# Kernel optimization log

Hardware: AMD Instinct MI355X
Metric: run time of the kernel (lower is better)

## Reference

```python
import jax, jax.numpy as jnp
import numpy as np

# Static config (matches init_kwargs)
H, G, D = 16, 4, 128          # n_head, n_query_groups, head_size
QPK = H // G                  # queries per kv group = 4
LEFT = 1024 - 1               # sliding-window left width (local_window-1)
SCALE = 1.0 / float(np.sqrt(D))
NEG = jnp.finfo(jnp.float32).min


def _rope(x, cos, sin):
    # x: [B,T,h,D]; cos/sin: [T, D/2]; non-interleaved (flash-attn) convention
    d2 = cos.shape[-1]
    x1, x2 = x[..., :d2], x[..., d2:]
    c = cos[None, :, None, :]
    s = sin[None, :, None, :]
    return jnp.concatenate([x1 * c - x2 * s, x1 * s + x2 * c], axis=-1)


def setup_inputs() -> dict:
    key = jax.random.key(0)
    ks = jax.random.split(key, 4)
    B, T, C = 1, 2048, 2048
    x = jax.random.normal(ks[0], (B, T, C), jnp.float32)
    # real RoPE tables, base 10000
    pos = jnp.arange(T, dtype=jnp.float32)
    inv_freq = 1.0 / (10000.0 ** (jnp.arange(0, D, 2, dtype=jnp.float32) / D))
    ang = pos[:, None] * inv_freq[None, :]        # [T, D/2]
    cos, sin = jnp.cos(ang), jnp.sin(ang)
    W_attn = jax.random.normal(ks[1], ((H + 2 * G) * D, C), jnp.float32) * 0.02
    W_proj = jax.random.normal(ks[2], (C, H * D), jnp.float32) * 0.02
    k_sink = jax.random.normal(ks[3], (G * D,), jnp.float32) * 0.02
    v_sink = jnp.zeros((G * D,), jnp.float32)     # buffer, zeros in original
    return {"x": x, "cos": cos, "sin": sin, "W_attn": W_attn,
            "W_proj": W_proj, "k_sink": k_sink, "v_sink": v_sink}


def reference(x, cos, sin, W_attn, W_proj, k_sink, v_sink):
    B, T, C = x.shape
    # fused QKV projection (no bias)
    qkv = jnp.einsum('btc,oc->bto', x, W_attn)                 # [B,T,(H+2G)*D]
    qkv = qkv.reshape(B, T, G, QPK + 2, D)
    q = qkv[:, :, :, :QPK, :].reshape(B, T, H, D)              # [B,T,H,D]
    k = qkv[:, :, :, QPK, :]                                   # [B,T,G,D]
    v = qkv[:, :, :, QPK + 1, :]                               # [B,T,G,D]
    # RoPE on q and k
    q = _rope(q, cos, sin)
    k = _rope(k, cos, sin)
    # prepend sink token to k/v -> seqlen_k = T+1
    k = jnp.concatenate([jnp.broadcast_to(k_sink.reshape(1, 1, G, D), (B, 1, G, D)), k], axis=1)
    v = jnp.concatenate([jnp.broadcast_to(v_sink.reshape(1, 1, G, D), (B, 1, G, D)), v], axis=1)
    Tk = T + 1
    # GQA: group-major query head layout -> head h uses kv group h // QPK
    kh = jnp.repeat(k, QPK, axis=2)                            # [B,Tk,H,D]
    vh = jnp.repeat(v, QPK, axis=2)
    scores = jnp.einsum('bqhd,bkhd->bhqk', q, kh) * SCALE      # [B,H,T,Tk]
    # flash-attn causal + sliding window, bottom-right aligned: offset = Tk - T
    off = Tk - T
    i = jnp.arange(T)[:, None]
    j = jnp.arange(Tk)[None, :]
    allowed = (j <= i + off) & (j >= i + off - LEFT)
    scores = jnp.where(allowed[None, None], scores, NEG)
    p = jax.nn.softmax(scores, axis=-1)
    o = jnp.einsum('bhqk,bkhd->bqhd', p, vh).reshape(B, T, H * D)
    y = jnp.einsum('btd,cd->btc', o, W_proj)                   # output proj, no bias
    return y
```

## Files before the change

### kernel.cpp

```cpp
#include <hip/hip_runtime.h>

#define T_SEQ  2048
#define JP     2080
#define SL_F    0.12751744f
#define THR_L2  11.0f

typedef __attribute__((ext_vector_type(8))) short short8;
typedef __attribute__((ext_vector_type(4))) float f32x4;
typedef __attribute__((ext_vector_type(4))) int   i32x4;

__device__ __forceinline__ unsigned short f2bf(float f) {
  unsigned int u = __float_as_uint(f);
  u += 0x7fff + ((u >> 16) & 1);
  return (unsigned short)(u >> 16);
}

__device__ __forceinline__ void gload16(const void* g, void* l) {
  __builtin_amdgcn_global_load_lds(
      (const __attribute__((address_space(1))) void*)g,
      (__attribute__((address_space(3))) void*)l, 16, 0, 0);
}

__global__ __launch_bounds__(256) void quant3(
    const float* __restrict__ sx, signed char* __restrict__ dx, float* __restrict__ scx,
    const float* __restrict__ sa, signed char* __restrict__ da, float* __restrict__ sca,
    const float* __restrict__ sp, signed char* __restrict__ dp, float* __restrict__ scp) {
  __shared__ float red[4];
  int r = blockIdx.x;
  const float* s; signed char* d; float* sc; int p;
  if (r < 2048)      { s = sx; d = dx; sc = scx; p = 4194304; }
  else if (r < 5120) { r -= 2048; s = sa; d = da; sc = sca; p = 6291456; }
  else               { r -= 5120; s = sp; d = dp; sc = scp; p = 4194304; }
  const int tid = threadIdx.x;
  const float4* spv = (const float4*)(s + (size_t)r * 2048) + tid * 2;
  float4 v0 = spv[0], v1 = spv[1];
  float vv[8] = {v0.x, v0.y, v0.z, v0.w, v1.x, v1.y, v1.z, v1.w};
  float am = 0.f;
#pragma unroll
  for (int e = 0; e < 8; ++e) am = fmaxf(am, fabsf(vv[e]));
#pragma unroll
  for (int o = 1; o <= 32; o <<= 1) am = fmaxf(am, __shfl_xor(am, o, 64));
  if ((tid & 63) == 0) red[tid >> 6] = am;
  __syncthreads();
  am = fmaxf(fmaxf(red[0], red[1]), fmaxf(red[2], red[3]));
  const float inv = (am > 1e-30f) ? 32512.f / am : 0.f;
  if (tid == 0) sc[r] = am * (1.f / 32512.f);
  int hb[8], lb[8];
#pragma unroll
  for (int e = 0; e < 8; ++e) {
    int n  = __float2int_rn(vv[e] * inv);
    int nh = (n + 128) >> 8;
    hb[e] = nh & 0xff;
    lb[e] = (n - (nh << 8)) & 0xff;
  }
  int2 hw, lw;
  hw.x = hb[0] | (hb[1] << 8) | (hb[2] << 16) | (hb[3] << 24);
  hw.y = hb[4] | (hb[5] << 8) | (hb[6] << 16) | (hb[7] << 24);
  lw.x = lb[0] | (lb[1] << 8) | (lb[2] << 16) | (lb[3] << 24);
  lw.y = lb[4] | (lb[5] << 8) | (lb[6] << 16) | (lb[7] << 24);
  *(int2*)(d + (size_t)r * 2048 + tid * 8)     = hw;
  *(int2*)(d + p + (size_t)r * 2048 + tid * 8) = lw;
}

__global__ __launch_bounds__(256, 2) void gemm_i8(const signed char* __restrict__ Ag,
                                                  const signed char* __restrict__ Bg,
                                                  const float* __restrict__ sav,
                                                  const float* __restrict__ sbv,
                                                  float* __restrict__ C,
                                                  int M, int N, int K,
                                                  int kLen, int saUniform, int useAtomic) {
  __shared__ signed char Anh[2][128 * 64], Anl[2][128 * 64];
  __shared__ signed char Bnh[2][128 * 64], Bnl[2][128 * 64];

  const int tid  = threadIdx.x;
  const int lane = tid & 63;
  const int wid  = tid >> 6;
  const int wm   = (wid >> 1) << 6;
  const int wn   = (wid & 1) << 6;
  const int lo16 = lane & 15;
  const int hi4  = lane >> 4;
  const int m0   = blockIdx.y << 7;
  const int n0   = blockIdx.x << 7;
  const int kOff = blockIdx.z * kLen;
  const size_t MK = (size_t)M * K;
  const size_t NK = (size_t)N * K;

  const int r0 = (wid << 4) + (lane >> 2);
  const int r1 = r0 + 64;
  const int cB = (lane & 3) << 4;
  const signed char* a0g = Ag + (size_t)(m0 + r0) * K + cB + kOff;
  const signed char* a1g = Ag + (size_t)(m0 + r1) * K + cB + kOff;
  const signed char* b0g = Bg + (size_t)(n0 + r0) * K + cB + kOff;
  const signed char* b1g = Bg + (size_t)(n0 + r1) * K + cB + kOff;
  const int o0 = wid << 10;
  const int o1 = (4 + wid) << 10;

  int ra[4], rb[4];
#pragma unroll
  for (int i = 0; i < 4; ++i) {
    ra[i] = ((wm + i * 16 + lo16) << 6) + (hi4 << 4);
    rb[i] = ((wn + i * 16 + lo16) << 6) + (hi4 << 4);
  }

  i32x4 acc1[4][4], acc2[4][4];
  const i32x4 zi = {0, 0, 0, 0};
#pragma unroll
  for (int i = 0; i < 4; ++i)
#pragma unroll
    for (int j = 0; j < 4; ++j) { acc1[i][j] = zi; acc2[i][j] = zi; }

  gload16(a0g,      &Anh[0][o0]);
  gload16(a1g,      &Anh[0][o1]);
  gload16(a0g + MK, &Anl[0][o0]);
  gload16(a1g + MK, &Anl[0][o1]);
  gload16(b0g,      &Bnh[0][o0]);
  gload16(b1g,      &Bnh[0][o1]);
  gload16(b0g + NK, &Bnl[0][o0]);
  gload16(b1g + NK, &Bnl[0][o1]);

  int cur = 0;
  for (int k0 = 0; k0 < kLen; k0 += 64) {
    const bool more = (k0 + 64) < kLen;
    if (more) {
      const int nxt = cur ^ 1;
      const int kn  = k0 + 64;
      gload16(a0g + kn,      &Anh[nxt][o0]);
      gload16(a1g + kn,      &Anh[nxt][o1]);
      gload16(a0g + MK + kn, &Anl[nxt][o0]);
      gload16(a1g + MK + kn, &Anl[nxt][o1]);
      gload16(b0g + kn,      &Bnh[nxt][o0]);
      gload16(b1g + kn,      &Bnh[nxt][o1]);
      gload16(b0g + NK + kn, &Bnl[nxt][o0]);
      gload16(b1g + NK + kn, &Bnl[nxt][o1]);
      asm volatile("s_waitcnt vmcnt(8)" ::: "memory");
    } else {
      asm volatile("s_waitcnt vmcnt(0)" ::: "memory");
    }
    __builtin_amdgcn_s_barrier();
    __builtin_amdgcn_sched_barrier(0);

    i32x4 fah[4], fal[4], fbh[4], fbl[4];
#pragma unroll
    for (int i = 0; i < 4; ++i) {
      fah[i] = *(const i32x4*)&Anh[cur][ra[i]];
      fal[i] = *(const i32x4*)&Anl[cur][ra[i]];
      fbh[i] = *(const i32x4*)&Bnh[cur][rb[i]];
      fbl[i] = *(const i32x4*)&Bnl[cur][rb[i]];
    }
#pragma unroll
    for (int i = 0; i < 4; ++i)
#pragma unroll
      for (int j = 0; j < 4; ++j) {
        acc1[i][j] = __builtin_amdgcn_mfma_i32_16x16x64_i8(fah[i], fbh[j], acc1[i][j], 0, 0, 0);
        acc2[i][j] = __builtin_amdgcn_mfma_i32_16x16x64_i8(fah[i], fbl[j], acc2[i][j], 0, 0, 0);
        acc2[i][j] = __builtin_amdgcn_mfma_i32_16x16x64_i8(fal[i], fbh[j], acc2[i][j], 0, 0, 0);
      }

    __builtin_amdgcn_sched_barrier(0);
    __builtin_amdgcn_s_barrier();
    asm volatile("" ::: "memory");
    cur ^= 1;
  }

  const float saU = saUniform ? sav[0] : 0.f;
#pragma unroll
  for (int i = 0; i < 4; ++i) {
    const int rowb = m0 + wm + i * 16 + (hi4 << 2);
    float sa0, sa1, sa2, sa3;
    if (saUniform) { sa0 = sa1 = sa2 = sa3 = saU; }
    else { sa0 = sav[rowb]; sa1 = sav[rowb + 1]; sa2 = sav[rowb + 2]; sa3 = sav[rowb + 3]; }
#pragma unroll
    for (int j = 0; j < 4; ++j) {
      const int col = n0 + wn + j * 16 + lo16;
      const float sb = sbv[col];
      float* cp = C + (size_t)rowb * N + col;
      float v0 = fmaf(65536.f, (float)acc1[i][j][0], 256.f * (float)acc2[i][j][0]) * sa0 * sb;
      float v1 = fmaf(65536.f, (float)acc1[i][j][1], 256.f * (float)acc2[i][j][1]) * sa1 * sb;
      float v2 = fmaf(65536.f, (float)acc1[i][j][2], 256.f * (float)acc2[i][j][2]) * sa2 * sb;
      float v3 = fmaf(65536.f, (float)acc1[i][j][3], 256.f * (float)acc2[i][j][3]) * sa3 * sb;
      if (useAtomic) {
        atomicAdd(cp, v0);
        atomicAdd(cp + (size_t)N, v1);
        atomicAdd(cp + (size_t)2 * N, v2);
        atomicAdd(cp + (size_t)3 * N, v3);
      } else {
        cp[0]           = v0;
        cp[(size_t)N]   = v1;
        cp[(size_t)2*N] = v2;
        cp[(size_t)3*N] = v3;
      }
    }
  }
}

#define RB_Q  4096
#define RB_K  1024
#define RB_KE 64
#define RB_V  65

__global__ __launch_bounds__(256) void rope2(const float* __restrict__ qkv,
                                             const float* __restrict__ cosb,
                                             const float* __restrict__ sinb,
                                             const float* __restrict__ ksink,
                                             const float* __restrict__ vsink,
                                             unsigned short* __restrict__ qb,
                                             unsigned short* __restrict__ kb,
                                             unsigned short* __restrict__ vtb,
                                             float* __restrict__ vamax) {
  __shared__ unsigned short tl[512 * 33];
  __shared__ float vred[4];
  const int bid = blockIdx.x, tid = threadIdx.x;
  if (bid < RB_Q) {
    int idx = bid * 256 + tid;
    int t = idx >> 9, rem = idx & 511;
    int h = rem >> 5, dp = (rem & 31) << 1;
    int g = h >> 2, qi = h & 3;
    const float* src = qkv + (size_t)t * 3072 + g * 768 + qi * 128;
    float2 x1 = *(const float2*)(src + dp);
    float2 x2 = *(const float2*)(src + 64 + dp);
    float2 c  = *(const float2*)(cosb + t * 64 + dp);
    float2 s  = *(const float2*)(sinb + t * 64 + dp);
    ushort2 o1 = { f2bf(x1.x * c.x - x2.x * s.x), f2bf(x1.y * c.y - x2.y * s.y) };
    ushort2 o2 = { f2bf(x1.x * s.x + x2.x * c.x), f2bf(x1.y * s.y + x2.y * c.y) };
    *(ushort2*)(qb + (size_t)t * 2048 + h * 128 + dp)      = o1;
    *(ushort2*)(qb + (size_t)t * 2048 + h * 128 + 64 + dp) = o2;
  } else if (bid < RB_Q + RB_K) {
    int idx = (bid - RB_Q) * 256 + tid;
    int t = idx >> 7, rem = idx & 127;
    int g = rem >> 5, dp = (rem & 31) << 1;
    const float* src = qkv + (size_t)t * 3072 + g * 768 + 512;
    float2 x1 = *(const float2*)(src + dp);
    float2 x2 = *(const float2*)(src + 64 + dp);
    float2 c  = *(const float2*)(cosb + t * 64 + dp);
    float2 s  = *(const float2*)(sinb + t * 64 + dp);
    ushort2 o1 = { f2bf(x1.x * c.x - x2.x * s.x), f2bf(x1.y * c.y - x2.y * s.y) };
    ushort2 o2 = { f2bf(x1.x * s.x + x2.x * c.x), f2bf(x1.y * s.y + x2.y * c.y) };
    size_t base = (size_t)(t + 1) * 512 + g * 128 + dp;
    *(ushort2*)(kb + base)      = o1;
    *(ushort2*)(kb + base + 64) = o2;
  } else if (bid < RB_Q + RB_K + RB_KE) {
    int idx = (bid - RB_Q - RB_K) * 256 + tid;
    int jj = idx >> 9, c = idx & 511;
    if (jj == 0) kb[c] = f2bf(ksink[c]);
    else         kb[(size_t)(2048 + jj) * 512 + c] = 0;
  } else {
    int b  = bid - RB_Q - RB_K - RB_KE;
    int j0 = b << 5;
    float am = 0.f;
#pragma unroll 4
    for (int st = 0; st < 64; ++st) {
      int id = st * 256 + tid;
      int jj = id >> 9, c = id & 511;
      int j = j0 + jj;
      float val;
      if (j == 0)          val = vsink[c];
      else if (j <= T_SEQ) val = qkv[(size_t)(j - 1) * 3072 + (c >> 7) * 768 + 640 + (c & 127)];
      else                 val = 0.f;
      am = fmaxf(am, fabsf(val));
      tl[c * 33 + jj] = f2bf(val);
    }
#pragma unroll
    for (int o = 1; o <= 32; o <<= 1) am = fmaxf(am, __shfl_xor(am, o, 64));
    if ((tid & 63) == 0) vred[tid >> 6] = am;
    __syncthreads();
    if (tid == 0)
      vamax[b] = fmaxf(fmaxf(vred[0], vred[1]), fmaxf(vred[2], vred[3]));
#pragma unroll 4
    for (int st = 0; st < 32; ++st) {
      int id = st * 256 + tid;
      int row = id >> 4, jp = (id & 15) << 1;
      ushort2 w = { tl[row * 33 + jp], tl[row * 33 + jp + 1] };
      *(ushort2*)(vtb + (size_t)row * JP + j0 + jp) = w;
    }
  }
}

#define KSTR 136
#define VSTR 40

__global__ __launch_bounds__(512) void attn_mfma_bf16(const unsigned short* __restrict__ qb,
                                                      const unsigned short* __restrict__ kb,
                                                      const unsigned short* __restrict__ vtb,
                                                      signed char* __restrict__ ops,
                                                      const float* __restrict__ vamax,
                                                      float* __restrict__ s_oq) {
  __shared__ unsigned short Kl[2][32 * KSTR];
  __shared__ unsigned short Vl[2][128 * VSTR];

  const int bid  = blockIdx.x;
  const int tid  = threadIdx.x;
  const int tile = bid >> 2;
  const int g    = bid & 3;
  const int t0b  = tile << 5;
  const int wv   = tid >> 6;
  const int hq   = wv & 3;
  const int sub  = wv >> 2;
  const int h    = g * 4 + hq;
  const int lane = tid & 63;
  const int lo   = lane & 15;
  const int hi   = lane >> 4;
  const int t0w  = t0b + (sub << 4);
  const int t    = t0w + lo;

  float vam = 0.f;
  for (int i = lane; i < 65; i += 64) vam = fmaxf(vam, vamax[i]);
#pragma unroll
  for (int o = 1; o <= 32; o <<= 1) vam = fmaxf(vam, __shfl_xor(vam, o, 64));
  const float s_eff = vam * 1.00390625f;
  const float invq  = (vam > 1e-30f) ? 32512.f / s_eff : 0.f;
  if (bid == 0 && tid == 0) *s_oq = s_eff * (1.f / 32512.f);

  const int sj   = tid >> 4;
  const int sc   = (tid & 15) << 3;
  const int kphi = ((((sj & 7) << 2) | (sj >> 3))) * KSTR + sc;
  const int svd  = tid >> 2;
  const int svj  = (tid & 3) << 3;
  const int vdst = svd * VSTR + svj;
  const unsigned short* ksrc = kb  + (size_t)sj * 512 + g * 128 + sc;
  const unsigned short* vsrc = vtb + (size_t)(g * 128 + svd) * JP + svj;

  short8 qfrag[4];
  {
    const unsigned short* qp = qb + (size_t)t * 2048 + h * 128 + (hi << 3);
#pragma unroll
    for (int d0 = 0; d0 < 4; ++d0) qfrag[d0] = *(const short8*)(qp + d0 * 32);
  }

  f32x4 acc[8];
  const f32x4 z4 = {0.f, 0.f, 0.f, 0.f};
#pragma unroll
  for (int dt = 0; dt < 8; ++dt) acc[dt] = z4;

  float m = -1e4f, l = 0.f;

  int jlo = t0b - 1022; if (jlo < 0) jlo = 0;
  const int jb0  = jlo & ~31;
  const int jmax = t0b + 32;
  const int nch  = ((jmax - jb0) >> 5) + 1;

  const int klA = (((lo & 3) << 2) | (lo >> 2)) * KSTR + (hi << 3);

  uint4 kreg = *(const uint4*)(ksrc + (size_t)jb0 * 512);
  uint4 vreg = *(const uint4*)(vsrc + jb0);
  *(uint4*)&Kl[0][kphi] = kreg;
  *(uint4*)&Vl[0][vdst] = vreg;
  __syncthreads();

  int bsel = 0;
  for (int ci = 0; ci < nch; ++ci) {
    const int jb = jb0 + (ci << 5);
    const bool more = (ci + 1 < nch);
    if (more) {
      const int jn = jb + 32;
      kreg = *(const uint4*)(ksrc + (size_t)jn * 512);
      vreg = *(const uint4*)(vsrc + jn);
    }

    const unsigned short* Kb = &Kl[bsel][0];
    f32x4 sa = z4, sb = z4;
#pragma unroll
    for (int d0 = 0; d0 < 4; ++d0) {
      short8 ka  = *(const short8*)(Kb + klA + d0 * 32);
      short8 kB2 = *(const short8*)(Kb + klA + 16 * KSTR + d0 * 32);
      sa = __builtin_amdgcn_mfma_f32_16x16x32_bf16(ka,  qfrag[d0], sa, 0, 0, 0);
      sb = __builtin_amdgcn_mfma_f32_16x16x32_bf16(kB2, qfrag[d0], sb, 0, 0, 0);
    }

    float z[8];
    const int jbase = jb + (hi << 3);
    const bool interior = (jb >= t0w - 1007) && (jb <= t0w - 30);
    if (interior) {
#pragma unroll
      for (int r = 0; r < 4; ++r) { z[r] = sa[r] * SL_F; z[r + 4] = sb[r] * SL_F; }
    } else {
#pragma unroll
      for (int r = 0; r < 8; ++r) {
        float sv = (r < 4) ? sa[r] : sb[r - 4];
        int j = jbase + r;
        bool valid = (j <= t + 1) && (j >= t - 1022);
        z[r] = valid ? sv * SL_F : -1e30f;
      }
    }

    float lmax = fmaxf(fmaxf(fmaxf(z[0], z[1]), fmaxf(z[2], z[3])),
                       fmaxf(fmaxf(z[4], z[5]), fmaxf(z[6], z[7])));
    if (!__all(lmax <= m + THR_L2)) {
      float cm = lmax;
      cm = fmaxf(cm, __shfl_xor(cm, 16, 64));
      cm = fmaxf(cm, __shfl_xor(cm, 32, 64));
      float mn = fmaxf(m, cm);
      float a  = exp2f(m - mn);
      l *= a;
#pragma unroll
      for (int dt = 0; dt < 8; ++dt) acc[dt] *= a;
      m = mn;
    }

    float p[8];
#pragma unroll
    for (int r = 0; r < 8; ++r) { p[r] = exp2f(z[r] - m); l += p[r]; }

    short8 pfrag;
#pragma unroll
    for (int e = 0; e < 8; ++e) pfrag[e] = (short)f2bf(p[e]);

    const unsigned short* Vb = &Vl[bsel][0];
#pragma unroll
    for (int dt = 0; dt < 8; ++dt) {
      short8 vf = *(const short8*)(Vb + (dt * 16 + lo) * VSTR + (hi << 3));
      acc[dt] = __builtin_amdgcn_mfma_f32_16x16x32_bf16(vf, pfrag, acc[dt], 0, 0, 0);
    }

    if (more) {
      *(uint4*)&Kl[bsel ^ 1][kphi] = kreg;
      *(uint4*)&Vl[bsel ^ 1][vdst] = vreg;
      __syncthreads();
      bsel ^= 1;
    }
  }

  float lt = l;
  lt += __shfl_xor(lt, 16, 64);
  lt += __shfl_xor(lt, 32, 64);
  const float inv = 1.f / lt;

  const size_t elem = (size_t)t * 2048 + h * 128 + (hi << 2);
#pragma unroll
  for (int dt = 0; dt < 8; ++dt) {
    f32x4 o4 = acc[dt] * inv;
    int hb[4], lb[4];
#pragma unroll
    for (int e = 0; e < 4; ++e) {
      int n  = __float2int_rn(o4[e] * invq);
      int nh = (n + 128) >> 8;
      hb[e] = nh & 0xff;
      lb[e] = (n - (nh << 8)) & 0xff;
    }
    int hw = hb[0] | (hb[1] << 8) | (hb[2] << 16) | (hb[3] << 24);
    int lw = lb[0] | (lb[1] << 8) | (lb[2] << 16) | (lb[3] << 24);
    *(int*)(ops + elem + dt * 16)           = hw;
    *(int*)(ops + 4194304 + elem + dt * 16) = lw;
  }
}

extern "C" void kernel_launch(void* const* d_in, const int* in_sizes, int n_in,
                              void* d_out, int out_size, void* d_ws, size_t ws_size,
                              hipStream_t stream) {
  const float* x     = (const float*)d_in[0];
  const float* cosb  = (const float*)d_in[1];
  const float* sinb  = (const float*)d_in[2];
  const float* Wa    = (const float*)d_in[3];
  const float* Wp    = (const float*)d_in[4];
  const float* ksink = (const float*)d_in[5];
  const float* vsink = (const float*)d_in[6];
  float* y = (float*)d_out;

  char* ws = (char*)d_ws;
  float*          qkv = (float*)ws;
  signed char*    ops = (signed char*)ws;
  signed char*    xs  = (signed char*)(ws + 25165824);
  unsigned short* qb  = (unsigned short*)(ws + 25165824);
  signed char*    was = (signed char*)(ws + 34214432);
  unsigned short* kbb = (unsigned short*)(ws + 34214432);
  unsigned short* vtb = (unsigned short*)(ws + 36344352);
  signed char*    wps = (signed char*)(ws + 46797344);
  float*          s_x   = (float*)(ws + 55185952);
  float*          s_wa  = (float*)(ws + 55194144);
  float*          s_wp  = (float*)(ws + 55206432);
  float*          vamax = (float*)(ws + 55214624);
  float*          s_oq  = (float*)(ws + 55215136);

  hipMemsetAsync(y, 0, out_size, stream);
  quant3<<<7168, 256, 0, stream>>>(x, xs, s_x, Wa, was, s_wa, Wp, wps, s_wp);
  gemm_i8<<<dim3(24, 16, 1), 256, 0, stream>>>(xs, was, s_x, s_wa, qkv,
                                               2048, 3072, 2048, 2048, 0, 0);
  rope2<<<RB_Q + RB_K + RB_KE + RB_V, 256, 0, stream>>>(qkv, cosb, sinb, ksink, vsink,
                                                        qb, kbb, vtb, vamax);
  attn_mfma_bf16<<<256, 512, 0, stream>>>(qb, kbb, vtb, ops, vamax, s_oq);
  gemm_i8<<<dim3(16, 16, 2), 256, 0, stream>>>(ops, wps, s_oq, s_wp, y,
                                               2048, 2048, 2048, 1024, 1, 1);
}
```

Before: 284.2 us.

## Drop split-K atomics in output GEMM and halve attention query tile per block

The output projection GEMM no longer splits K across two z-slices with atomicAdd into a memset output. It now runs a single full-K pass with plain stores, which removes the memset and the atomic traffic but halves the number of blocks. The attention kernel moves from 512-thread blocks covering 32 queries to 256-thread blocks covering 16 queries, doubling the grid to 512 blocks. Each thread now loads two K/V slices per chunk so one block still fills the shared tiles. This trades more redundant K/V loading across blocks for better occupancy and load balance.

```diff
diff --git a/kernel.cpp b/kernel.cpp
--- a/kernel.cpp
+++ b/kernel.cpp
@@ -67,8 +67,7 @@
                                                   const float* __restrict__ sav,
                                                   const float* __restrict__ sbv,
                                                   float* __restrict__ C,
-                                                  int M, int N, int K,
-                                                  int kLen, int saUniform, int useAtomic) {
+                                                  int M, int N, int K, int saUniform) {
   __shared__ signed char Anh[2][128 * 64], Anl[2][128 * 64];
   __shared__ signed char Bnh[2][128 * 64], Bnl[2][128 * 64];
 
@@ -81,17 +80,16 @@
   const int hi4  = lane >> 4;
   const int m0   = blockIdx.y << 7;
   const int n0   = blockIdx.x << 7;
-  const int kOff = blockIdx.z * kLen;
   const size_t MK = (size_t)M * K;
   const size_t NK = (size_t)N * K;
 
   const int r0 = (wid << 4) + (lane >> 2);
   const int r1 = r0 + 64;
   const int cB = (lane & 3) << 4;
-  const signed char* a0g = Ag + (size_t)(m0 + r0) * K + cB + kOff;
-  const signed char* a1g = Ag + (size_t)(m0 + r1) * K + cB + kOff;
-  const signed char* b0g = Bg + (size_t)(n0 + r0) * K + cB + kOff;
-  const signed char* b1g = Bg + (size_t)(n0 + r1) * K + cB + kOff;
+  const signed char* a0g = Ag + (size_t)(m0 + r0) * K + cB;
+  const signed char* a1g = Ag + (size_t)(m0 + r1) * K + cB;
+  const signed char* b0g = Bg + (size_t)(n0 + r0) * K + cB;
+  const signed char* b1g = Bg + (size_t)(n0 + r1) * K + cB;
   const int o0 = wid << 10;
   const int o1 = (4 + wid) << 10;
 
@@ -119,8 +117,8 @@
   gload16(b1g + NK, &Bnl[0][o1]);
 
   int cur = 0;
-  for (int k0 = 0; k0 < kLen; k0 += 64) {
-    const bool more = (k0 + 64) < kLen;
+  for (int k0 = 0; k0 < K; k0 += 64) {
+    const bool more = (k0 + 64) < K;
     if (more) {
       const int nxt = cur ^ 1;
       const int kn  = k0 + 64;
@@ -174,21 +172,10 @@
       const int col = n0 + wn + j * 16 + lo16;
       const float sb = sbv[col];
       float* cp = C + (size_t)rowb * N + col;
-      float v0 = fmaf(65536.f, (float)acc1[i][j][0], 256.f * (float)acc2[i][j][0]) * sa0 * sb;
-      float v1 = fmaf(65536.f, (float)acc1[i][j][1], 256.f * (float)acc2[i][j][1]) * sa1 * sb;
-      float v2 = fmaf(65536.f, (float)acc1[i][j][2], 256.f * (float)acc2[i][j][2]) * sa2 * sb;
-      float v3 = fmaf(65536.f, (float)acc1[i][j][3], 256.f * (float)acc2[i][j][3]) * sa3 * sb;
-      if (useAtomic) {
-        atomicAdd(cp, v0);
-        atomicAdd(cp + (size_t)N, v1);
-        atomicAdd(cp + (size_t)2 * N, v2);
-        atomicAdd(cp + (size_t)3 * N, v3);
-      } else {
-        cp[0]           = v0;
-        cp[(size_t)N]   = v1;
-        cp[(size_t)2*N] = v2;
-        cp[(size_t)3*N] = v3;
-      }
+      cp[0]           = fmaf(65536.f, (float)acc1[i][j][0], 256.f * (float)acc2[i][j][0]) * sa0 * sb;
+      cp[(size_t)N]   = fmaf(65536.f, (float)acc1[i][j][1], 256.f * (float)acc2[i][j][1]) * sa1 * sb;
+      cp[(size_t)2*N] = fmaf(65536.f, (float)acc1[i][j][2], 256.f * (float)acc2[i][j][2]) * sa2 * sb;
+      cp[(size_t)3*N] = fmaf(65536.f, (float)acc1[i][j][3], 256.f * (float)acc2[i][j][3]) * sa3 * sb;
     }
   }
 }
@@ -278,7 +265,7 @@
 #define KSTR 136
 #define VSTR 40
 
-__global__ __launch_bounds__(512) void attn_mfma_bf16(const unsigned short* __restrict__ qb,
+__global__ __launch_bounds__(256) void attn_mfma_bf16(const unsigned short* __restrict__ qb,
                                                       const unsigned short* __restrict__ kb,
                                                       const unsigned short* __restrict__ vtb,
                                                       signed char* __restrict__ ops,
@@ -291,16 +278,13 @@
   const int tid  = threadIdx.x;
   const int tile = bid >> 2;
   const int g    = bid & 3;
-  const int t0b  = tile << 5;
+  const int t0b  = tile << 4;
   const int wv   = tid >> 6;
-  const int hq   = wv & 3;
-  const int sub  = wv >> 2;
-  const int h    = g * 4 + hq;
+  const int h    = g * 4 + wv;
   const int lane = tid & 63;
   const int lo   = lane & 15;
   const int hi   = lane >> 4;
-  const int t0w  = t0b + (sub << 4);
-  const int t    = t0w + lo;
+  const int t    = t0b + lo;
 
   float vam = 0.f;
   for (int i = lane; i < 65; i += 64) vam = fmaxf(vam, vamax[i]);
@@ -312,12 +296,16 @@
 
   const int sj   = tid >> 4;
   const int sc   = (tid & 15) << 3;
-  const int kphi = ((((sj & 7) << 2) | (sj >> 3))) * KSTR + sc;
+  const int kphi0 = ((((sj      & 7) << 2) | ( sj       >> 3))) * KSTR + sc;
+  const int kphi1 = ((((sj      & 7) << 2) | ((sj + 16) >> 3))) * KSTR + sc;
   const int svd  = tid >> 2;
   const int svj  = (tid & 3) << 3;
-  const int vdst = svd * VSTR + svj;
-  const unsigned short* ksrc = kb  + (size_t)sj * 512 + g * 128 + sc;
-  const unsigned short* vsrc = vtb + (size_t)(g * 128 + svd) * JP + svj;
+  const int vdst0 = svd * VSTR + svj;
+  const int vdst1 = (svd + 64) * VSTR + svj;
+  const unsigned short* ksrc0 = kb  + (size_t)sj * 512 + g * 128 + sc;
+  const unsigned short* ksrc1 = kb  + (size_t)(sj + 16) * 512 + g * 128 + sc;
+  const unsigned short* vsrc0 = vtb + (size_t)(g * 128 + svd) * JP + svj;
+  const unsigned short* vsrc1 = vtb + (size_t)(g * 128 + svd + 64) * JP + svj;
 
   short8 qfrag[4];
   {
@@ -335,15 +323,19 @@
 
   int jlo = t0b - 1022; if (jlo < 0) jlo = 0;
   const int jb0  = jlo & ~31;
-  const int jmax = t0b + 32;
+  const int jmax = t0b + 16;
   const int nch  = ((jmax - jb0) >> 5) + 1;
 
   const int klA = (((lo & 3) << 2) | (lo >> 2)) * KSTR + (hi << 3);
 
-  uint4 kreg = *(const uint4*)(ksrc + (size_t)jb0 * 512);
-  uint4 vreg = *(const uint4*)(vsrc + jb0);
-  *(uint4*)&Kl[0][kphi] = kreg;
-  *(uint4*)&Vl[0][vdst] = vreg;
+  uint4 kr0 = *(const uint4*)(ksrc0 + (size_t)jb0 * 512);
+  uint4 kr1 = *(const uint4*)(ksrc1 + (size_t)jb0 * 512);
+  uint4 vr0 = *(const uint4*)(vsrc0 + jb0);
+  uint4 vr1 = *(const uint4*)(vsrc1 + jb0);
+  *(uint4*)&Kl[0][kphi0] = kr0;
+  *(uint4*)&Kl[0][kphi1] = kr1;
+  *(uint4*)&Vl[0][vdst0] = vr0;
+  *(uint4*)&Vl[0][vdst1] = vr1;
   __syncthreads();
 
   int bsel = 0;
@@ -352,8 +344,10 @@
     const bool more = (ci + 1 < nch);
     if (more) {
       const int jn = jb + 32;
-      kreg = *(const uint4*)(ksrc + (size_t)jn * 512);
-      vreg = *(const uint4*)(vsrc + jn);
+      kr0 = *(const uint4*)(ksrc0 + (size_t)jn * 512);
+      kr1 = *(const uint4*)(ksrc1 + (size_t)jn * 512);
+      vr0 = *(const uint4*)(vsrc0 + jn);
+      vr1 = *(const uint4*)(vsrc1 + jn);
     }
 
     const unsigned short* Kb = &Kl[bsel][0];
@@ -368,7 +362,7 @@
 
     float z[8];
     const int jbase = jb + (hi << 3);
-    const bool interior = (jb >= t0w - 1007) && (jb <= t0w - 30);
+    const bool interior = (jb >= t0b - 1007) && (jb <= t0b - 30);
     if (interior) {
 #pragma unroll
       for (int r = 0; r < 4; ++r) { z[r] = sa[r] * SL_F; z[r + 4] = sb[r] * SL_F; }
@@ -412,8 +406,10 @@
     }
 
     if (more) {
-      *(uint4*)&Kl[bsel ^ 1][kphi] = kreg;
-      *(uint4*)&Vl[bsel ^ 1][vdst] = vreg;
+      *(uint4*)&Kl[bsel ^ 1][kphi0] = kr0;
+      *(uint4*)&Kl[bsel ^ 1][kphi1] = kr1;
+      *(uint4*)&Vl[bsel ^ 1][vdst0] = vr0;
+      *(uint4*)&Vl[bsel ^ 1][vdst1] = vr1;
       __syncthreads();
       bsel ^= 1;
     }
@@ -470,13 +466,12 @@
   float*          vamax = (float*)(ws + 55214624);
   float*          s_oq  = (float*)(ws + 55215136);
 
-  hipMemsetAsync(y, 0, out_size, stream);
   quant3<<<7168, 256, 0, stream>>>(x, xs, s_x, Wa, was, s_wa, Wp, wps, s_wp);
-  gemm_i8<<<dim3(24, 16, 1), 256, 0, stream>>>(xs, was, s_x, s_wa, qkv,
-                                               2048, 3072, 2048, 2048, 0, 0);
+  gemm_i8<<<dim3(24, 16), 256, 0, stream>>>(xs, was, s_x, s_wa, qkv,
+                                            2048, 3072, 2048, 0);
   rope2<<<RB_Q + RB_K + RB_KE + RB_V, 256, 0, stream>>>(qkv, cosb, sinb, ksink, vsink,
                                                         qb, kbb, vtb, vamax);
-  attn_mfma_bf16<<<256, 512, 0, stream>>>(qb, kbb, vtb, ops, vamax, s_oq);
-  gemm_i8<<<dim3(16, 16, 2), 256, 0, stream>>>(ops, wps, s_oq, s_wp, y,
-                                               2048, 2048, 2048, 1024, 1, 1);
-}
+  attn_mfma_bf16<<<512, 256, 0, stream>>>(qb, kbb, vtb, ops, vamax, s_oq);
+  gemm_i8<<<dim3(16, 16), 256, 0, stream>>>(ops, wps, s_oq, s_wp, y,
+                                            2048, 2048, 2048, 1);
+}
```

After: 287.5 us. Within noise of the previous version (+1.2%).
